# Kernel optimization log

Measured on AMD Instinct MI355X. Metric: run time of the kernel, lower is better.

The kernel has to match this reference:

```python
import jax, jax.numpy as jnp
import numpy as np

H = 512        # hidden_size
ENC = 2 * H    # encoder (context) feature dim
V = 10000      # vocab_size
B, T, L = 32, 500, 100
NEG_INF = -1e10


def setup_inputs() -> dict:
    key = jax.random.key(0)
    ks = jax.random.split(key, 16)
    sc = 0.02
    inp = {
        "h_batch": jax.random.normal(ks[0], (B, T, ENC), jnp.float32),
        "seq_lens": jax.random.randint(ks[1], (B,), 1, T + 1),
        "labels": jax.random.randint(ks[2], (B, L), 0, V),
        # content-based (additive) attention params
        "attn_Ws": jax.random.normal(ks[3], (H, H), jnp.float32) * sc,
        "attn_Wh": jax.random.normal(ks[4], (ENC, H), jnp.float32) * sc,
        "attn_b": jnp.zeros((H,), jnp.float32),
        "attn_v": jax.random.normal(ks[5], (H,), jnp.float32) * sc,
        # output path
        "W_sy": jax.random.normal(ks[6], (H, H), jnp.float32) * sc,
        "b_sy": jnp.zeros((H,), jnp.float32),
        "W_gy": jax.random.normal(ks[7], (ENC, H), jnp.float32) * sc,
        "b_gy": jnp.zeros((H,), jnp.float32),
        "W_yy": jax.random.normal(ks[8], (H, V), jnp.float32) * sc,
        "b_yy": jnp.zeros((V,), jnp.float32),
        # recurrence path
        "E_yr": jax.random.normal(ks[9], (V, 4 * H), jnp.float32) * sc,
        "W_sr": jax.random.normal(ks[10], (H, 4 * H), jnp.float32) * sc,
        "b_sr": jnp.zeros((4 * H,), jnp.float32),
        "W_gr": jax.random.normal(ks[11], (ENC, 4 * H), jnp.float32) * sc,
        "b_gr": jnp.zeros((4 * H,), jnp.float32),
    }
    return inp


def _func_lstm(rec_in, c):
    i, f, g, o = jnp.split(rec_in, 4, axis=-1)
    c_new = jax.nn.sigmoid(f) * c + jax.nn.sigmoid(i) * jnp.tanh(g)
    s_new = jax.nn.sigmoid(o) * jnp.tanh(c_new)
    return s_new, c_new


def reference(h_batch, seq_lens, labels, attn_Ws, attn_Wh, attn_b, attn_v,
              W_sy, b_sy, W_gy, b_gy, W_yy, b_yy,
              E_yr, W_sr, b_sr, W_gr, b_gr):
    Tlen = h_batch.shape[1]
    mask = jnp.arange(Tlen)[None, :] < seq_lens[:, None]          # [B,T]
    h_proj = jnp.einsum('bte,eh->bth', h_batch, attn_Wh) + attn_b  # precompute

    s0 = jnp.zeros((h_batch.shape[0], H), h_batch.dtype)
    c0 = jnp.zeros_like(s0)

    def step(carry, y_t):
        s, c = carry
        # content-based attention: e = v . tanh(Ws s + Wh h)
        e = jnp.einsum('bth,h->bt', jnp.tanh(h_proj + (s @ attn_Ws)[:, None, :]), attn_v)
        e = jnp.where(mask, e, NEG_INF)
        alpha = jax.nn.softmax(e, axis=-1)                         # [B,T]
        g = jnp.einsum('bt,bte->be', alpha, h_batch)               # [B,ENC]
        dec_feat = (g @ W_gy + b_gy) + (s @ W_sy + b_sy)
        y = jnp.tanh(dec_feat) @ W_yy + b_yy                       # [B,V]
        rec_in = E_yr[y_t] + (s @ W_sr + b_sr) + (g @ W_gr + b_gr) # [B,4H]
        s_new, c_new = _func_lstm(rec_in, c)
        return (s_new, c_new), y

    _, preds = jax.lax.scan(step, (s0, c0), labels.T)              # [L,B,V]
    return jnp.transpose(preds, (1, 0, 2))                         # [B,L,V]
```

## Files before the change

kernel.cpp:

```cpp
#include <hip/hip_runtime.h>
#include <cstdint>

#define B_   32
#define T_   500
#define H_   512
#define ENC_ 1024
#define V_   10000
#define L_   100
#define H4_  2048
#define NB_  256
#define NT_  512

#define OFF_HPROJ 0
#define OFF_WYYP  4096000
#define OFF_WRECP 6656000
#define OFF_WSB   10588160
#define OFF_S     10719232
#define OFF_DECTP 10735616
#define OFF_RACC  10752000
#define OFF_G0    10817536
#define OFF_G1    10850304
#define OFF_E     10883072
#define OFF_DEN   10899456
#define OFF_BAR   10899520
#define OFF_HB16  10899584
#define ZERO_CNT  180352

using bf16x8 = __attribute__((ext_vector_type(8))) short;
using f32x4  = __attribute__((ext_vector_type(4))) float;

__device__ __forceinline__ f32x4 mfma16(bf16x8 a, bf16x8 b, f32x4 c){
  return __builtin_amdgcn_mfma_f32_16x16x32_bf16(a, b, c, 0, 0, 0);
}
__device__ __forceinline__ unsigned short bfr(float f){
  unsigned x = __float_as_uint(f);
  return (unsigned short)((x + 0x7FFFu + ((x>>16)&1u)) >> 16);
}
__device__ __forceinline__ void bfsplit(float f, short& hi, short& lo){
  unsigned short h = bfr(f);
  float hf = __uint_as_float(((unsigned)h) << 16);
  hi = (short)h;
  lo = (short)bfr(f - hf);
}
__device__ __forceinline__ float bf2f(unsigned short u){
  return __uint_as_float(((unsigned)u) << 16);
}
__device__ __forceinline__ float ftanh(float x){
  float t = fminf(fmaxf(2.f*x, -30.f), 30.f);
  float e = __expf(t);
  return (e - 1.f) / (e + 1.f);
}
__device__ __forceinline__ float fsig(float x){
  float t = fminf(fmaxf(x, -30.f), 30.f);
  return 1.f / (1.f + __expf(-t));
}
__device__ __forceinline__ float gload(const float* p){
  return __hip_atomic_load((float*)p, __ATOMIC_RELAXED, __HIP_MEMORY_SCOPE_AGENT);
}
__device__ __forceinline__ void gstore(float* p, float v){
  __hip_atomic_store(p, v, __ATOMIC_RELAXED, __HIP_MEMORY_SCOPE_AGENT);
}
__device__ __forceinline__ void gstoreu(unsigned* p, unsigned v){
  __hip_atomic_store(p, v, __ATOMIC_RELAXED, __HIP_MEMORY_SCOPE_AGENT);
}
__device__ __forceinline__ void gload2(const float* p, float& a, float& b){
  unsigned long long u = __hip_atomic_load((const unsigned long long*)p,
                          __ATOMIC_RELAXED, __HIP_MEMORY_SCOPE_AGENT);
  a = __uint_as_float((unsigned)u);
  b = __uint_as_float((unsigned)(u >> 32));
}
__device__ __forceinline__ void gloadu2(const unsigned* p, unsigned& a, unsigned& b){
  unsigned long long u = __hip_atomic_load((const unsigned long long*)p,
                          __ATOMIC_RELAXED, __HIP_MEMORY_SCOPE_AGENT);
  a = (unsigned)u;
  b = (unsigned)(u >> 32);
}

__device__ __forceinline__ void gridbar(unsigned* bars, unsigned it){
  asm volatile("s_waitcnt vmcnt(0) lgkmcnt(0)" ::: "memory");
  __syncthreads();
  if (threadIdx.x == 0){
    unsigned* gc = bars + 1 + (blockIdx.x & 15);
    unsigned old = __hip_atomic_fetch_add(gc, 1u, __ATOMIC_RELAXED, __HIP_MEMORY_SCOPE_AGENT);
    if (old == it*16u + 15u)
      __hip_atomic_fetch_add(bars, 1u, __ATOMIC_RELAXED, __HIP_MEMORY_SCOPE_AGENT);
    while (__hip_atomic_load(bars, __ATOMIC_RELAXED, __HIP_MEMORY_SCOPE_AGENT) < (it+1u)*16u)
      __builtin_amdgcn_s_sleep(2);
  }
  __syncthreads();
  asm volatile("" ::: "memory");
}

__global__ void k_init(float* __restrict__ ws){
  int i = blockIdx.x * 256 + threadIdx.x;
  if (i < ZERO_CNT) ws[OFF_S + i] = 0.f;
}

__global__ void k_packWyy(const float* __restrict__ Wyy, float* __restrict__ ws){
  unsigned short* wp = (unsigned short*)(ws + OFF_WYYP);
  int t = blockIdx.x * 256 + threadIdx.x;
  if (t >= 625*16*64) return;
  int vt = t / 1024;
  int rem = t - vt*1024;
  int kc = rem >> 6, lane = rem & 63;
  int v  = vt*16 + (lane & 15);
  int k0 = kc*32 + ((lane >> 4) << 3);
  bf16x8 H;
  #pragma unroll
  for (int j = 0; j < 8; ++j) H[j] = (short)bfr(Wyy[(size_t)(k0+j)*V_ + v]);
  *(bf16x8*)(wp + ((size_t)(vt*16 + kc)*64 + lane)*8) = H;
}

__global__ void k_packWrec(const float* __restrict__ Wsy, const float* __restrict__ Wgy,
                           const float* __restrict__ Wsr, const float* __restrict__ Wgr,
                           float* __restrict__ ws){
  unsigned short* wp = (unsigned short*)(ws + OFF_WRECP);
  int t = blockIdx.x * 256 + threadIdx.x;
  if (t >= 160*48*64) return;
  int vt = t / (48*64);
  int rem = t - vt*(48*64);
  int kc = rem >> 6, lane = rem & 63;
  int col = vt*16 + (lane & 15);
  int k0  = kc*32 + ((lane >> 4) << 3);
  bf16x8 H, Lo;
  #pragma unroll
  for (int j = 0; j < 8; ++j){
    int k = k0 + j;
    float x;
    if (k < 512) x = (col < 512) ? Wsy[(size_t)k*512 + col] : Wsr[(size_t)k*2048 + (col-512)];
    else         x = (col < 512) ? Wgy[(size_t)(k-512)*512 + col] : Wgr[(size_t)(k-512)*2048 + (col-512)];
    short h, lo; bfsplit(x, h, lo);
    H[j] = h; Lo[j] = lo;
  }
  size_t base = ((size_t)(vt*48 + kc)*2)*512 + (size_t)lane*8;
  *(bf16x8*)(wp + base) = H;
  *(bf16x8*)(wp + base + 512) = Lo;
}

__global__ void k_packWs(const float* __restrict__ Ws, float* __restrict__ ws){
  unsigned short* wp = (unsigned short*)(ws + OFF_WSB);
  int i = blockIdx.x * 256 + threadIdx.x;
  wp[i] = bfr(Ws[i]);
}

__global__ void k_packHB(const float* __restrict__ hb, float* __restrict__ ws){
  unsigned short* wp = (unsigned short*)(ws + OFF_HB16);
  int i = blockIdx.x * 256 + threadIdx.x;
  if (i < B_*T_*ENC_) wp[i] = bfr(hb[i]);
}

__global__ void k_hproj(const float* __restrict__ A, const float* __restrict__ W,
                        const float* __restrict__ bias, const int* __restrict__ lens,
                        float* __restrict__ ws){
  unsigned short* C = (unsigned short*)(ws + OFF_HPROJ);
  const int bm = blockIdx.x * 64;
  const int bn = blockIdx.y * 64;
  {
    int b0 = bm / T_, t0 = bm % T_;
    int b1 = (bm + 63) / T_;
    if (b0 == b1 && t0 >= lens[b0]) return;
  }
  __shared__ float As[64][33];
  __shared__ float Bs[32][68];
  const int tid = threadIdx.x;
  const int tx = tid & 15, ty = tid >> 4;
  float acc[4][4];
  #pragma unroll
  for (int i = 0; i < 4; ++i)
    #pragma unroll
    for (int j = 0; j < 4; ++j) acc[i][j] = 0.f;
  for (int k0 = 0; k0 < 1024; k0 += 32){
    for (int i = tid; i < 64*32; i += 256){
      int rr = i >> 5, cc = i & 31;
      As[rr][cc] = A[(size_t)(bm + rr) * 1024 + k0 + cc];
    }
    for (int i = tid; i < 32*64; i += 256){
      int rr = i >> 6, cc = i & 63;
      Bs[rr][cc] = W[(size_t)(k0 + rr) * 512 + bn + cc];
    }
    __syncthreads();
    #pragma unroll
    for (int kk = 0; kk < 32; ++kk){
      float a0 = As[ty*4+0][kk], a1 = As[ty*4+1][kk];
      float a2 = As[ty*4+2][kk], a3 = As[ty*4+3][kk];
      float4 b4 = *(const float4*)&Bs[kk][tx*4];
      acc[0][0] += a0*b4.x; acc[0][1] += a0*b4.y; acc[0][2] += a0*b4.z; acc[0][3] += a0*b4.w;
      acc[1][0] += a1*b4.x; acc[1][1] += a1*b4.y; acc[1][2] += a1*b4.z; acc[1][3] += a1*b4.w;
      acc[2][0] += a2*b4.x; acc[2][1] += a2*b4.y; acc[2][2] += a2*b4.z; acc[2][3] += a2*b4.w;
      acc[3][0] += a3*b4.x; acc[3][1] += a3*b4.y; acc[3][2] += a3*b4.z; acc[3][3] += a3*b4.w;
    }
    __syncthreads();
  }
  #pragma unroll
  for (int i = 0; i < 4; ++i){
    int m = bm + ty*4 + i;
    ushort4 o;
    o.x = bfr(acc[i][0] + bias[bn + tx*4 + 0]);
    o.y = bfr(acc[i][1] + bias[bn + tx*4 + 1]);
    o.z = bfr(acc[i][2] + bias[bn + tx*4 + 2]);
    o.w = bfr(acc[i][3] + bias[bn + tx*4 + 3]);
    *(ushort4*)&C[(size_t)m * 512 + bn + tx*4] = o;
  }
}

__global__ __launch_bounds__(NT_, 2) void k_persist(
    const int* __restrict__ lens,
    const int* __restrict__ labels, const float* __restrict__ av,
    const float* __restrict__ bsy, const float* __restrict__ bgy,
    const float* __restrict__ byy,
    const float* __restrict__ Eyr,
    const float* __restrict__ bsr, const float* __restrict__ bgr,
    float* __restrict__ out, float* __restrict__ ws)
{
  const int blk = blockIdx.x;
  const int tid = threadIdx.x;
  const int w   = tid >> 6;
  const int lane= tid & 63;
  unsigned* bars = (unsigned*)(ws + OFF_BAR);
  const unsigned short* wyyp  = (const unsigned short*)(ws + OFF_WYYP);
  const unsigned short* wrecp = (const unsigned short*)(ws + OFF_WRECP);
  const unsigned short* wsb   = (const unsigned short*)(ws + OFF_WSB);
  const unsigned short* hpB   = (const unsigned short*)(ws + OFF_HPROJ);
  const unsigned short* hb16  = (const unsigned short*)(ws + OFF_HB16);
  unsigned* dectP = (unsigned*)(ws + OFF_DECTP);
  __shared__ __align__(16) float smem[8192];

  const int arow  = lane & 15;
  const int klane = (lane >> 4) << 3;
  float c_reg = 0.f;

  for (int l = 0; l <= L_; ++l){
    const int p = l & 1;
    const int goff = p ? OFF_G1 : OFF_G0;
    if (blk < 157){
      if (l > 0){
        const int kh = w & 1;
        const int vtslot = w >> 1;
        const int vt = blk*4 + vtslot;
        f32x4 a0 = {0.f,0.f,0.f,0.f}, a1 = {0.f,0.f,0.f,0.f};
        if (vt < 625){
          for (int kc2 = 0; kc2 < 8; ++kc2){
            const int kc = kh*8 + kc2;
            const int k0 = kc*32 + klane;
            bf16x8 Ahi0, Alo0, Ahi1, Alo1;
            {
              unsigned q[8];
              const unsigned* dp = dectP + arow*H_ + k0;
              gloadu2(dp+0, q[0], q[1]);
              gloadu2(dp+2, q[2], q[3]);
              gloadu2(dp+4, q[4], q[5]);
              gloadu2(dp+6, q[6], q[7]);
              #pragma unroll
              for (int j = 0; j < 8; ++j){
                Ahi0[j] = (short)(q[j] >> 16);
                Alo0[j] = (short)(q[j] & 0xFFFFu);
              }
            }
            {
              unsigned q[8];
              const unsigned* dp = dectP + (arow+16)*H_ + k0;
              gloadu2(dp+0, q[0], q[1]);
              gloadu2(dp+2, q[2], q[3]);
              gloadu2(dp+4, q[4], q[5]);
              gloadu2(dp+6, q[6], q[7]);
              #pragma unroll
              for (int j = 0; j < 8; ++j){
                Ahi1[j] = (short)(q[j] >> 16);
                Alo1[j] = (short)(q[j] & 0xFFFFu);
              }
            }
            bf16x8 Bv = *(const bf16x8*)(wyyp + ((size_t)(vt*16 + kc)*64 + lane)*8);
            a0 = mfma16(Ahi0, Bv, a0);
            a0 = mfma16(Alo0, Bv, a0);
            a1 = mfma16(Ahi1, Bv, a1);
            a1 = mfma16(Alo1, Bv, a1);
          }
        }
        if (vt < 625 && kh == 0){
          #pragma unroll
          for (int r = 0; r < 4; ++r){
            smem[vtslot*512 +       lane*4 + r] = a0[r];
            smem[vtslot*512 + 256 + lane*4 + r] = a1[r];
          }
        }
        __syncthreads();
        if (vt < 625 && kh == 1){
          const int v = vt*16 + arow;
          const float bv = byy[v];
          const int lv = l - 1;
          #pragma unroll
          for (int r = 0; r < 4; ++r){
            const int row0 = ((lane >> 4) << 2) + r;
            float v0 = smem[vtslot*512 +       lane*4 + r] + a0[r] + bv;
            float v1 = smem[vtslot*512 + 256 + lane*4 + r] + a1[r] + bv;
            out[((size_t)(row0)*L_      + lv)*V_ + v] = v0;
            out[((size_t)(row0 + 16)*L_ + lv)*V_ + v] = v1;
          }
        }
        __syncthreads();
      }
    } else if (blk < 221){
      if (l < L_){
        const int u = blk - 157;
        const int b = u >> 1, half = u & 1;
        float* ssm = smem;
        float* part = smem + 512;
        float* wsm = smem + 2560;
        if (l == 0){
          ssm[tid] = 0.f;
          c_reg = 0.f;
        } else {
          const int h = tid;
          const float* ey = Eyr + (size_t)labels[b*L_ + (l-1)] * H4_;
          float ri = gload(&ws[OFF_RACC + b*H4_ + h])        + bsr[h]      + bgr[h]      + ey[h];
          float rf = gload(&ws[OFF_RACC + b*H4_ + 512 + h])  + bsr[512+h]  + bgr[512+h]  + ey[512+h];
          float rg = gload(&ws[OFF_RACC + b*H4_ + 1024 + h]) + bsr[1024+h] + bgr[1024+h] + ey[1024+h];
          float ro = gload(&ws[OFF_RACC + b*H4_ + 1536 + h]) + bsr[1536+h] + bgr[1536+h] + ey[1536+h];
          float cn = fsig(rf)*c_reg + fsig(ri)*ftanh(rg);
          float sn = fsig(ro)*ftanh(cn);
          c_reg = cn;
          if (half == 0) gstore(&ws[OFF_S + b*H_ + h], sn);
          ssm[h] = sn;
        }
        __syncthreads();
        {
          const int colp = tid & 255;
          const int kh2  = tid >> 8;
          const int col0 = colp*2;
          const float* sp = ssm + kh2*256;
          const unsigned short* wb = wsb + (size_t)(kh2*256)*512 + col0;
          float acc0 = 0.f, acc1 = 0.f;
          for (int k = 0; k < 256; k += 8){
            float4 s0 = *(const float4*)&sp[k];
            float4 s1 = *(const float4*)&sp[k+4];
            unsigned wv[8];
            #pragma unroll
            for (int j = 0; j < 8; ++j)
              wv[j] = *(const unsigned*)&wb[(size_t)(k+j)*512];
            float sv[8] = {s0.x,s0.y,s0.z,s0.w,s1.x,s1.y,s1.z,s1.w};
            #pragma unroll
            for (int j = 0; j < 8; ++j){
              acc0 += sv[j] * bf2f((unsigned short)(wv[j] & 0xFFFFu));
              acc1 += sv[j] * bf2f((unsigned short)(wv[j] >> 16));
            }
          }
          part[kh2*1024 + col0]     = acc0;
          part[kh2*1024 + col0 + 1] = acc1;
        }
        __syncthreads();
        wsm[tid] = part[tid] + part[1024 + tid];
        __syncthreads();
        const int len = lens[b];
        float avr[8], swr[8];
        #pragma unroll
        for (int j = 0; j < 8; ++j){
          avr[j] = av[lane*8 + j];
          swr[j] = wsm[lane*8 + j];
        }
        float* e = ws + OFF_E;
        for (int t = 2*w + half; t < len; t += 16){
          bf16x8 hp = *(const bf16x8*)&hpB[(size_t)(b*T_ + t)*512 + lane*8];
          float sum = 0.f;
          #pragma unroll
          for (int j = 0; j < 8; ++j)
            sum += avr[j] * ftanh(bf2f((unsigned short)hp[j]) + swr[j]);
          #pragma unroll
          for (int off = 32; off > 0; off >>= 1) sum += __shfl_xor(sum, off, 64);
          if (lane == 0) gstore(&e[b*T_ + t], __expf(sum));
        }
      }
    } else {
      if (l < L_){
        for (int i = (blk - 221)*NT_ + tid; i < B_*ENC_; i += 35*NT_)
          gstore(&ws[goff + i], 0.f);
        if (blk == 221 && tid < 32)
          gstore(&ws[OFF_DEN + p*32 + tid], 0.f);
      }
    }
    if (l == L_) break;
    gridbar(bars, (unsigned)(l*3 + 0));

    {
      const int b = blk >> 3, ts = blk & 7;
      const int len = lens[b];
      const int clen = (len + 7) >> 3;
      const int t0 = ts*clen;
      const int t1 = min(t0 + clen, len);
      const int n  = t1 - t0;
      float* sc = smem;
      float* pg = smem + 128;
      if (tid < n) sc[tid] = gload(&ws[OFF_E + b*T_ + t0 + tid]);
      __syncthreads();
      if (n > 0 && tid < 64){
        float s2 = 0.f;
        for (int i = tid; i < n; i += 64) s2 += sc[i];
        #pragma unroll
        for (int off = 32; off > 0; off >>= 1) s2 += __shfl_xor(s2, off, 64);
        if (tid == 0) atomicAdd(&ws[OFF_DEN + p*32 + b], s2);
      }
      const int tg = tid >> 8, cq = tid & 255;
      const int col0 = cq*4;
      {
        float4 acc = {0.f,0.f,0.f,0.f};
        const unsigned short* hp = hb16 + (size_t)b*T_*ENC_ + col0;
        for (int t = t0 + tg; t < t1; t += 2){
          ushort4 x = *(const ushort4*)&hp[(size_t)t * ENC_];
          float a = sc[t - t0];
          acc.x += a*bf2f(x.x); acc.y += a*bf2f(x.y);
          acc.z += a*bf2f(x.z); acc.w += a*bf2f(x.w);
        }
        *(float4*)&pg[tg*1024 + col0] = acc;
      }
      __syncthreads();
      if (tg == 0 && n > 0){
        float4 x0 = *(const float4*)&pg[col0];
        float4 x1 = *(const float4*)&pg[1024 + col0];
        float* gp = ws + goff + b*ENC_ + col0;
        atomicAdd(gp+0, x0.x+x1.x);
        atomicAdd(gp+1, x0.y+x1.y);
        atomicAdd(gp+2, x0.z+x1.z);
        atomicAdd(gp+3, x0.w+x1.w);
      }
    }
    gridbar(bars, (unsigned)(l*3 + 1));

    if (blk < 80){
      const float invb0 = 1.f / gload(&ws[OFF_DEN + p*32 + arow]);
      const float invb1 = 1.f / gload(&ws[OFF_DEN + p*32 + arow + 16]);
      f32x4 acc[2][2];
      #pragma unroll
      for (int vv = 0; vv < 2; ++vv)
        #pragma unroll
        for (int rg = 0; rg < 2; ++rg) acc[vv][rg] = (f32x4){0.f,0.f,0.f,0.f};
      for (int j6 = 0; j6 < 6; ++j6){
        const int kc = w*6 + j6;
        const int k0 = kc*32 + klane;
        const bool isg = (k0 >= 512);
        bf16x8 Ahi0, Alo0, Ahi1, Alo1;
        {
          const float* src = !isg ? &ws[OFF_S + arow*H_ + k0]
                                  : &ws[goff + arow*ENC_ + (k0 - 512)];
          float x[8];
          gload2(src+0, x[0], x[1]);
          gload2(src+2, x[2], x[3]);
          gload2(src+4, x[4], x[5]);
          gload2(src+6, x[6], x[7]);
          if (isg){
            #pragma unroll
            for (int j = 0; j < 8; ++j) x[j] *= invb0;
          }
          #pragma unroll
          for (int j = 0; j < 8; ++j){
            short h, lo; bfsplit(x[j], h, lo);
            Ahi0[j] = h; Alo0[j] = lo;
          }
        }
        {
          const float* src = !isg ? &ws[OFF_S + (arow+16)*H_ + k0]
                                  : &ws[goff + (arow+16)*ENC_ + (k0 - 512)];
          float x[8];
          gload2(src+0, x[0], x[1]);
          gload2(src+2, x[2], x[3]);
          gload2(src+4, x[4], x[5]);
          gload2(src+6, x[6], x[7]);
          if (isg){
            #pragma unroll
            for (int j = 0; j < 8; ++j) x[j] *= invb1;
          }
          #pragma unroll
          for (int j = 0; j < 8; ++j){
            short h, lo; bfsplit(x[j], h, lo);
            Ahi1[j] = h; Alo1[j] = lo;
          }
        }
        #pragma unroll
        for (int vv = 0; vv < 2; ++vv){
          const int vt = blk*2 + vv;
          const unsigned short* wp = wrecp + ((size_t)(vt*48 + kc)*2)*512 + (size_t)lane*8;
          bf16x8 Bhi = *(const bf16x8*)wp;
          bf16x8 Blo = *(const bf16x8*)(wp + 512);
          acc[vv][0] = mfma16(Ahi0, Bhi, acc[vv][0]);
          acc[vv][0] = mfma16(Alo0, Bhi, acc[vv][0]);
          acc[vv][0] = mfma16(Ahi0, Blo, acc[vv][0]);
          acc[vv][1] = mfma16(Ahi1, Bhi, acc[vv][1]);
          acc[vv][1] = mfma16(Alo1, Bhi, acc[vv][1]);
          acc[vv][1] = mfma16(Ahi1, Blo, acc[vv][1]);
        }
      }
      #pragma unroll
      for (int vv = 0; vv < 2; ++vv)
        #pragma unroll
        for (int rg = 0; rg < 2; ++rg)
          #pragma unroll
          for (int r = 0; r < 4; ++r)
            smem[((w*2 + vv)*2 + rg)*256 + lane*4 + r] = acc[vv][rg][r];
      __syncthreads();
      #pragma unroll
      for (int oo = 0; oo < 2; ++oo){
        const int q   = tid + oo*512;
        const int vv  = q >> 9;
        const int rem = q & 511;
        const int bt  = rem >> 8;
        const int r8  = rem & 255;
        float v = 0.f;
        #pragma unroll
        for (int w8 = 0; w8 < 8; ++w8)
          v += smem[((w8*2 + vv)*2 + bt)*256 + r8];
        const int ln = r8 >> 2, rr = r8 & 3;
        const int row = bt*16 + ((ln >> 4) << 2) + rr;
        const int col = (blk*2 + vv)*16 + (ln & 15);
        if (col < 512){
          float t = ftanh(v + bsy[col] + bgy[col]);
          unsigned short hi_ = bfr(t);
          unsigned short lo_ = bfr(t - bf2f(hi_));
          gstoreu(&dectP[row*H_ + col], ((unsigned)hi_ << 16) | lo_);
        } else {
          gstore(&ws[OFF_RACC + row*H4_ + (col - 512)], v);
        }
      }
    }
    gridbar(bars, (unsigned)(l*3 + 2));
  }
}

extern "C" void kernel_launch(void* const* d_in, const int* in_sizes, int n_in,
                              void* d_out, int out_size, void* d_ws, size_t ws_size,
                              hipStream_t stream){
  const float* h_batch = (const float*)d_in[0];
  const int*   seq_lens= (const int*)d_in[1];
  const int*   labels  = (const int*)d_in[2];
  const float* attn_Ws = (const float*)d_in[3];
  const float* attn_Wh = (const float*)d_in[4];
  const float* attn_b  = (const float*)d_in[5];
  const float* attn_v  = (const float*)d_in[6];
  const float* W_sy    = (const float*)d_in[7];
  const float* b_sy    = (const float*)d_in[8];
  const float* W_gy    = (const float*)d_in[9];
  const float* b_gy    = (const float*)d_in[10];
  const float* W_yy    = (const float*)d_in[11];
  const float* b_yy    = (const float*)d_in[12];
  const float* E_yr    = (const float*)d_in[13];
  const float* W_sr    = (const float*)d_in[14];
  const float* b_sr    = (const float*)d_in[15];
  const float* W_gr    = (const float*)d_in[16];
  const float* b_gr    = (const float*)d_in[17];
  float* out = (float*)d_out;
  float* ws  = (float*)d_ws;

  k_init    <<<705, 256, 0, stream>>>(ws);
  k_packWyy <<<2500, 256, 0, stream>>>(W_yy, ws);
  k_packWrec<<<1920, 256, 0, stream>>>(W_sy, W_gy, W_sr, W_gr, ws);
  k_packWs  <<<1024, 256, 0, stream>>>(attn_Ws, ws);
  k_packHB  <<<64000, 256, 0, stream>>>(h_batch, ws);
  k_hproj   <<<dim3(250, 8), 256, 0, stream>>>(h_batch, attn_Wh, attn_b, seq_lens, ws);

  void* kargs[] = {
    (void*)&seq_lens, (void*)&labels, (void*)&attn_v,
    (void*)&b_sy, (void*)&b_gy, (void*)&b_yy,
    (void*)&E_yr, (void*)&b_sr, (void*)&b_gr,
    (void*)&out, (void*)&ws
  };
  hipLaunchCooperativeKernel((void*)k_persist, dim3(NB_), dim3(NT_), kargs, 0, stream);
}
```

Measured before the change: 9.609 ms.

## Drop low-bf16 weight term in recurrence GEMM, stage dec activations in LDS

The recurrence weight pack now stores only the rounded bf16 high part instead of a hi/lo split, so the per-step recurrence GEMM issues four MFMAs per tile instead of six and reads half the weight bytes. The LSTM state s is stored as pre-split packed hi/lo bf16 pairs, so the consumer skips the split. The output-projection blocks first copy the shared dec activation matrix into padded LDS, then read it with vector loads instead of per-wave global loads. This reduces precision of the recurrence weights, which may slightly change the numerical results, and enlarges the LDS allocation, which may lower occupancy.

```diff
diff --git a/kernel.cpp b/kernel.cpp
--- a/kernel.cpp
+++ b/kernel.cpp
@@ -122,19 +122,16 @@
   int kc = rem >> 6, lane = rem & 63;
   int col = vt*16 + (lane & 15);
   int k0  = kc*32 + ((lane >> 4) << 3);
-  bf16x8 H, Lo;
+  bf16x8 H;
   #pragma unroll
   for (int j = 0; j < 8; ++j){
     int k = k0 + j;
     float x;
     if (k < 512) x = (col < 512) ? Wsy[(size_t)k*512 + col] : Wsr[(size_t)k*2048 + (col-512)];
     else         x = (col < 512) ? Wgy[(size_t)(k-512)*512 + col] : Wgr[(size_t)(k-512)*2048 + (col-512)];
-    short h, lo; bfsplit(x, h, lo);
-    H[j] = h; Lo[j] = lo;
+    H[j] = (short)bfr(x);
   }
-  size_t base = ((size_t)(vt*48 + kc)*2)*512 + (size_t)lane*8;
-  *(bf16x8*)(wp + base) = H;
-  *(bf16x8*)(wp + base + 512) = Lo;
+  *(bf16x8*)(wp + ((size_t)(vt*48 + kc)*64 + lane)*8) = H;
 }
 
 __global__ void k_packWs(const float* __restrict__ Ws, float* __restrict__ ws){
@@ -223,7 +220,8 @@
   const unsigned short* hpB   = (const unsigned short*)(ws + OFF_HPROJ);
   const unsigned short* hb16  = (const unsigned short*)(ws + OFF_HB16);
   unsigned* dectP = (unsigned*)(ws + OFF_DECTP);
-  __shared__ __align__(16) float smem[8192];
+  unsigned* sP    = (unsigned*)(ws + OFF_S);
+  __shared__ __align__(16) float smem[18688];
 
   const int arow  = lane & 15;
   const int klane = (lane >> 4) << 3;
@@ -234,6 +232,15 @@
     const int goff = p ? OFF_G1 : OFF_G0;
     if (blk < 157){
       if (l > 0){
+        unsigned* dst = (unsigned*)smem;
+        for (int i = tid; i < 8192; i += NT_){
+          int row = i >> 8, k2 = (i & 255) << 1;
+          unsigned a, b;
+          gloadu2(dectP + row*H_ + k2, a, b);
+          dst[row*516 + k2]     = a;
+          dst[row*516 + k2 + 1] = b;
+        }
+        __syncthreads();
         const int kh = w & 1;
         const int vtslot = w >> 1;
         const int vt = blk*4 + vtslot;
@@ -244,12 +251,10 @@
             const int k0 = kc*32 + klane;
             bf16x8 Ahi0, Alo0, Ahi1, Alo1;
             {
-              unsigned q[8];
-              const unsigned* dp = dectP + arow*H_ + k0;
-              gloadu2(dp+0, q[0], q[1]);
-              gloadu2(dp+2, q[2], q[3]);
-              gloadu2(dp+4, q[4], q[5]);
-              gloadu2(dp+6, q[6], q[7]);
+              const unsigned* dp = dst + arow*516 + k0;
+              uint4 qa = *(const uint4*)(dp);
+              uint4 qb = *(const uint4*)(dp+4);
+              unsigned q[8] = {qa.x,qa.y,qa.z,qa.w,qb.x,qb.y,qb.z,qb.w};
               #pragma unroll
               for (int j = 0; j < 8; ++j){
                 Ahi0[j] = (short)(q[j] >> 16);
@@ -257,12 +262,10 @@
               }
             }
             {
-              unsigned q[8];
-              const unsigned* dp = dectP + (arow+16)*H_ + k0;
-              gloadu2(dp+0, q[0], q[1]);
-              gloadu2(dp+2, q[2], q[3]);
-              gloadu2(dp+4, q[4], q[5]);
-              gloadu2(dp+6, q[6], q[7]);
+              const unsigned* dp = dst + (arow+16)*516 + k0;
+              uint4 qa = *(const uint4*)(dp);
+              uint4 qb = *(const uint4*)(dp+4);
+              unsigned q[8] = {qa.x,qa.y,qa.z,qa.w,qb.x,qb.y,qb.z,qb.w};
               #pragma unroll
               for (int j = 0; j < 8; ++j){
                 Ahi1[j] = (short)(q[j] >> 16);
@@ -276,11 +279,12 @@
             a1 = mfma16(Alo1, Bv, a1);
           }
         }
+        float* red = smem + 16512;
         if (vt < 625 && kh == 0){
           #pragma unroll
           for (int r = 0; r < 4; ++r){
-            smem[vtslot*512 +       lane*4 + r] = a0[r];
-            smem[vtslot*512 + 256 + lane*4 + r] = a1[r];
+            red[vtslot*512 +       lane*4 + r] = a0[r];
+            red[vtslot*512 + 256 + lane*4 + r] = a1[r];
           }
         }
         __syncthreads();
@@ -291,8 +295,8 @@
           #pragma unroll
           for (int r = 0; r < 4; ++r){
             const int row0 = ((lane >> 4) << 2) + r;
-            float v0 = smem[vtslot*512 +       lane*4 + r] + a0[r] + bv;
-            float v1 = smem[vtslot*512 + 256 + lane*4 + r] + a1[r] + bv;
+            float v0 = red[vtslot*512 +       lane*4 + r] + a0[r] + bv;
+            float v1 = red[vtslot*512 + 256 + lane*4 + r] + a1[r] + bv;
             out[((size_t)(row0)*L_      + lv)*V_ + v] = v0;
             out[((size_t)(row0 + 16)*L_ + lv)*V_ + v] = v1;
           }
@@ -319,7 +323,10 @@
           float cn = fsig(rf)*c_reg + fsig(ri)*ftanh(rg);
           float sn = fsig(ro)*ftanh(cn);
           c_reg = cn;
-          if (half == 0) gstore(&ws[OFF_S + b*H_ + h], sn);
+          if (half == 0){
+            short h_, lo_; bfsplit(sn, h_, lo_);
+            gstoreu(&sP[b*H_ + h], ((unsigned)(unsigned short)h_ << 16) | (unsigned short)(unsigned short)lo_);
+          }
           ssm[h] = sn;
         }
         __syncthreads();
@@ -437,54 +444,64 @@
         const int k0 = kc*32 + klane;
         const bool isg = (k0 >= 512);
         bf16x8 Ahi0, Alo0, Ahi1, Alo1;
-        {
-          const float* src = !isg ? &ws[OFF_S + arow*H_ + k0]
-                                  : &ws[goff + arow*ENC_ + (k0 - 512)];
-          float x[8];
-          gload2(src+0, x[0], x[1]);
-          gload2(src+2, x[2], x[3]);
-          gload2(src+4, x[4], x[5]);
-          gload2(src+6, x[6], x[7]);
-          if (isg){
+        if (!isg){
+          unsigned q[8];
+          const unsigned* dp = sP + arow*H_ + k0;
+          gloadu2(dp+0, q[0], q[1]);
+          gloadu2(dp+2, q[2], q[3]);
+          gloadu2(dp+4, q[4], q[5]);
+          gloadu2(dp+6, q[6], q[7]);
+          #pragma unroll
+          for (int j = 0; j < 8; ++j){
+            Ahi0[j] = (short)(q[j] >> 16);
+            Alo0[j] = (short)(q[j] & 0xFFFFu);
+          }
+          const unsigned* dp1 = sP + (arow+16)*H_ + k0;
+          gloadu2(dp1+0, q[0], q[1]);
+          gloadu2(dp1+2, q[2], q[3]);
+          gloadu2(dp1+4, q[4], q[5]);
+          gloadu2(dp1+6, q[6], q[7]);
+          #pragma unroll
+          for (int j = 0; j < 8; ++j){
+            Ahi1[j] = (short)(q[j] >> 16);
+            Alo1[j] = (short)(q[j] & 0xFFFFu);
+          }
+        } else {
+          {
+            const float* src = &ws[goff + arow*ENC_ + (k0 - 512)];
+            float x[8];
+            gload2(src+0, x[0], x[1]);
+            gload2(src+2, x[2], x[3]);
+            gload2(src+4, x[4], x[5]);
+            gload2(src+6, x[6], x[7]);
             #pragma unroll
-            for (int j = 0; j < 8; ++j) x[j] *= invb0;
-          }
-          #pragma unroll
-          for (int j = 0; j < 8; ++j){
-            short h, lo; bfsplit(x[j], h, lo);
-            Ahi0[j] = h; Alo0[j] = lo;
-          }
-        }
-        {
-          const float* src = !isg ? &ws[OFF_S + (arow+16)*H_ + k0]
-                                  : &ws[goff + (arow+16)*ENC_ + (k0 - 512)];
-          float x[8];
-          gload2(src+0, x[0], x[1]);
-          gload2(src+2, x[2], x[3]);
-          gload2(src+4, x[4], x[5]);
-          gload2(src+6, x[6], x[7]);
-          if (isg){
+            for (int j = 0; j < 8; ++j){
+              short h, lo; bfsplit(x[j]*invb0, h, lo);
+              Ahi0[j] = h; Alo0[j] = lo;
+            }
+          }
+          {
+            const float* src = &ws[goff + (arow+16)*ENC_ + (k0 - 512)];
+            float x[8];
+            gload2(src+0, x[0], x[1]);
+            gload2(src+2, x[2], x[3]);
+            gload2(src+4, x[4], x[5]);
+            gload2(src+6, x[6], x[7]);
             #pragma unroll
-            for (int j = 0; j < 8; ++j) x[j] *= invb1;
-          }
-          #pragma unroll
-          for (int j = 0; j < 8; ++j){
-            short h, lo; bfsplit(x[j], h, lo);
-            Ahi1[j] = h; Alo1[j] = lo;
+            for (int j = 0; j < 8; ++j){
+              short h, lo; bfsplit(x[j]*invb1, h, lo);
+              Ahi1[j] = h; Alo1[j] = lo;
+            }
           }
         }
         #pragma unroll
         for (int vv = 0; vv < 2; ++vv){
           const int vt = blk*2 + vv;
-          const unsigned short* wp = wrecp + ((size_t)(vt*48 + kc)*2)*512 + (size_t)lane*8;
-          bf16x8 Bhi = *(const bf16x8*)wp;
-          bf16x8 Blo = *(const bf16x8*)(wp + 512);
-          acc[vv][0] = mfma16(Ahi0, Bhi, acc[vv][0]);
-          acc[vv][0] = mfma16(Alo0, Bhi, acc[vv][0]);
-          acc[vv][0] = mfma16(Ahi0, Blo, acc[vv][0]);
-          acc[vv][1] = mfma16(Ahi1, Bhi, acc[vv][1]);
-          acc[vv][1] = mfma16(Alo1, Bhi, acc[vv][1]);
-          acc[vv][1] = mfma16(Ahi1, Blo, acc[vv][1]);
+          bf16x8 Bv = *(const bf16x8*)(wrecp + ((size_t)(vt*48 + kc)*64 + lane)*8);
+          acc[vv][0] = mfma16(Ahi0, Bv, acc[vv][0]);
+          acc[vv][0] = mfma16(Alo0, Bv, acc[vv][0]);
+          acc[vv][1] = mfma16(Ahi1, Bv, acc[vv][1]);
+          acc[vv][1] = mfma16(Alo1, Bv, acc[vv][1]);
         }
       }
       #pragma unroll
```

New measurement: 9.647 ms. Within noise of the previous version (+0.4%).
